# Performance work log

Hardware: AMD Instinct MI355X
Metric: run time of the kernel (lower is better)

Reference implementation:

```python
import jax, jax.numpy as jnp
import numpy as np

B, L, H, NH = 4, 1024, 768, 12
NE, M, P = 30, 6, 600
EMB, BS, NC = 768, 16, 97
NEG = -1e30


def setup_inputs() -> dict:
    key = jax.random.key(0)
    ks = jax.random.split(key, 9)
    sequence_output = jax.random.normal(ks[0], (B, L, H), jnp.float32)
    attention = jax.random.uniform(ks[1], (B, NH, L, L), jnp.float32)
    mention_idx = jax.random.randint(ks[2], (B, NE, M), 0, L)
    mention_mask = jnp.ones((B, NE, M), jnp.float32)
    hts = jax.random.randint(ks[3], (B, P, 2), 0, NE)
    s = 0.02
    head_W = jax.random.normal(ks[4], (EMB, 2 * H), jnp.float32) * s
    head_b = jnp.zeros((EMB,), jnp.float32)
    tail_W = jax.random.normal(ks[5], (EMB, 2 * H), jnp.float32) * s
    tail_b = jnp.zeros((EMB,), jnp.float32)
    proj_W = jax.random.normal(ks[6], (H, EMB * BS), jnp.float32) * s
    cls_W = jax.random.normal(ks[7], (NC, H), jnp.float32) * s
    cls_b = jnp.zeros((NC,), jnp.float32)
    return {
        'sequence_output': sequence_output, 'attention': attention,
        'head_W': head_W, 'head_b': head_b, 'tail_W': tail_W, 'tail_b': tail_b,
        'proj_W': proj_W, 'cls_W': cls_W, 'cls_b': cls_b,
        'mention_mask': mention_mask, 'mention_idx': mention_idx, 'hts': hts,
    }


def reference(sequence_output, attention, head_W, head_b, tail_W, tail_b,
              proj_W, cls_W, cls_b, mention_mask, mention_idx, hts):
    b_, l_, h_ = sequence_output.shape
    bidx = jnp.arange(b_)[:, None, None]                     # [B,1,1]
    # ---- per-entity pooling (segment reduce over ragged mentions) ----
    m_emb = sequence_output[bidx, mention_idx]               # [B,NE,M,H]
    att_t = attention.transpose(0, 2, 1, 3)                  # [B,L,NH,L]
    m_att = att_t[bidx, mention_idx]                         # [B,NE,M,NH,L]
    masked = jnp.where(mention_mask[..., None] > 0, m_emb, NEG)
    e_emb = jax.nn.logsumexp(masked, axis=2)                 # [B,NE,H]
    cnt = jnp.maximum(mention_mask.sum(2), 1.0)              # [B,NE]
    e_att = (m_att * mention_mask[..., None, None]).sum(2) / cnt[..., None, None]  # [B,NE,NH,L]
    # ---- head/tail gathers over pairs ----
    b2 = jnp.arange(b_)[:, None]                             # [B,1]
    h_emb = e_emb[b2, hts[..., 0]]                           # [B,P,H]
    t_emb = e_emb[b2, hts[..., 1]]
    h_att = e_att[b2, hts[..., 0]]                           # [B,P,NH,L]
    t_att = e_att[b2, hts[..., 1]]
    ht_att = (h_att * t_att).mean(2)                         # [B,P,L]
    ht_att = ht_att / (ht_att.sum(-1, keepdims=True) + 1e-30)
    rs = jnp.einsum('bpl,blh->bph', ht_att, sequence_output) # [B,P,H]
    # ---- extractors + block-bilinear classifier ----
    hs = jnp.tanh(jnp.concatenate([h_emb, rs], -1) @ head_W.T + head_b)  # [B,P,EMB]
    ts = jnp.tanh(jnp.concatenate([t_emb, rs], -1) @ tail_W.T + tail_b)
    emb = hs.shape[-1]
    bs = proj_W.shape[1] // emb
    p_ = hs.shape[1]
    b1 = hs.reshape(b_, p_, emb // bs, bs)
    b2t = ts.reshape(b_, p_, emb // bs, bs)
    bl = (b1[..., :, None] * b2t[..., None, :]).reshape(b_, p_, emb * bs)
    logits = (bl @ proj_W.T) @ cls_W.T + cls_b               # [B,P,NC]
    return logits
```

## Files before the change

### kernel.cpp

```cpp
#include <hip/hip_runtime.h>
#include <cmath>

#define B_   4
#define L_   1024
#define H_   768
#define NH_  12
#define NE_  30
#define M_   6
#define P_   600
#define EMB_ 768
#define BS_  16
#define NC_  97

typedef __bf16 bf16x8 __attribute__((ext_vector_type(8)));
typedef float floatx4 __attribute__((ext_vector_type(4)));

union V16 { uint4 q; __bf16 b[8]; bf16x8 v; };
union V8  { unsigned long long u; __bf16 b[4]; };

__device__ __forceinline__ void gemm_core(
    const __bf16* __restrict__ A, int lda, long aRow0,
    const __bf16* __restrict__ Bt, int ldb, long bRow0,
    int K, __bf16* sm, floatx4 acc[2][2])
{
  const int tid = threadIdx.x;
  const int lid = tid & 63, w = tid >> 6;
  const int ar = (w & 1) * 32, bc = (w >> 1) * 32;
  const int frow = lid & 15, kg = lid >> 4;
  __bf16* As = sm;
  __bf16* Bs = sm + 64*40;
  const int srow = tid >> 2, skq = (tid & 3) * 8;
  const __bf16* ag = A + (aRow0 + srow) * (long)lda + skq;
  const __bf16* bg = Bt + (bRow0 + srow) * (long)ldb + skq;
  for (int k0 = 0; k0 < K; k0 += 32) {
    uint4 av = *reinterpret_cast<const uint4*>(ag + k0);
    uint4 bv = *reinterpret_cast<const uint4*>(bg + k0);
    __syncthreads();
    *reinterpret_cast<uint4*>(As + srow*40 + skq) = av;
    *reinterpret_cast<uint4*>(Bs + srow*40 + skq) = bv;
    __syncthreads();
    V16 a0, a1, b0, b1;
    a0.q = *reinterpret_cast<const uint4*>(As + (ar + frow)*40 + kg*8);
    a1.q = *reinterpret_cast<const uint4*>(As + (ar + 16 + frow)*40 + kg*8);
    b0.q = *reinterpret_cast<const uint4*>(Bs + (bc + frow)*40 + kg*8);
    b1.q = *reinterpret_cast<const uint4*>(Bs + (bc + 16 + frow)*40 + kg*8);
    acc[0][0] = __builtin_amdgcn_mfma_f32_16x16x32_bf16(a0.v, b0.v, acc[0][0], 0, 0, 0);
    acc[0][1] = __builtin_amdgcn_mfma_f32_16x16x32_bf16(a0.v, b1.v, acc[0][1], 0, 0, 0);
    acc[1][0] = __builtin_amdgcn_mfma_f32_16x16x32_bf16(a1.v, b0.v, acc[1][0], 0, 0, 0);
    acc[1][1] = __builtin_amdgcn_mfma_f32_16x16x32_bf16(a1.v, b1.v, acc[1][1], 0, 0, 0);
  }
}

#define S1_CVT  2400
#define S1_TPW  9216
#define S1_TPS  3072
#define S1_POOL 120
#define S1_ATT  1440

__device__ __forceinline__ void transpose_body(
    const float* __restrict__ in, __bf16* __restrict__ out,
    int R, int C, int bx, int by, float (*t)[33])
{
  int c0 = bx*32, r0 = by*32;
  int tx = threadIdx.x & 31, ty = threadIdx.x >> 5;
#pragma unroll
  for (int p = 0; p < 4; ++p)
    t[ty + p*8][tx] = in[(long)(r0 + ty + p*8)*C + c0 + tx];
  __syncthreads();
#pragma unroll
  for (int p = 0; p < 4; ++p)
    out[(long)(c0 + ty + p*8)*R + r0 + tx] = (__bf16)t[tx][ty + p*8];
}

__global__ __launch_bounds__(256) void k_prep(
    const float* __restrict__ seq, const float* __restrict__ att,
    const float* __restrict__ headW, const float* __restrict__ tailW,
    const float* __restrict__ projW, const float* __restrict__ clsW,
    const float* __restrict__ mmask, const int* __restrict__ midx,
    __bf16* __restrict__ Wt, __bf16* __restrict__ clsA,
    __bf16* __restrict__ projWT, __bf16* __restrict__ seqT,
    __bf16* __restrict__ e_embB, __bf16* __restrict__ e_att)
{
  __shared__ float t[32][33];
  int blk = blockIdx.x;
  int tid = threadIdx.x;
  if (blk < S1_CVT) {
    int gid = blk*256 + tid;
    if (gid < 2*H_*384) {
      int sel = gid / (H_*384);
      int rem = gid % (H_*384);
      int o = rem / 384;
      int k4 = (rem % 384) * 4;
      const float* W = sel ? tailW : headW;
      float4 v = *reinterpret_cast<const float4*>(W + (long)o*(2*H_) + k4);
      V8 d; d.b[0]=(__bf16)v.x; d.b[1]=(__bf16)v.y; d.b[2]=(__bf16)v.z; d.b[3]=(__bf16)v.w;
      *reinterpret_cast<unsigned long long*>(Wt + ((long)sel*H_ + o)*(2*H_) + k4) = d.u;
    } else {
      int rem = gid - 2*H_*384;
      int row = rem / 192;
      int k4 = (rem % 192) * 4;
      V8 d;
      if (row < NC_) {
        float4 v = *reinterpret_cast<const float4*>(clsW + (long)row*H_ + k4);
        d.b[0]=(__bf16)v.x; d.b[1]=(__bf16)v.y; d.b[2]=(__bf16)v.z; d.b[3]=(__bf16)v.w;
      } else {
        d.b[0]=d.b[1]=d.b[2]=d.b[3]=(__bf16)0.f;
      }
      *reinterpret_cast<unsigned long long*>(clsA + (long)row*H_ + k4) = d.u;
    }
  } else if (blk < S1_CVT + S1_TPW) {
    int b = blk - S1_CVT;
    transpose_body(projW, projWT, H_, EMB_*BS_, b % 384, b / 384, t);
  } else if (blk < S1_CVT + S1_TPW + S1_TPS) {
    int b = blk - (S1_CVT + S1_TPW);
    int bx = b % 24, by = (b / 24) % 32, bz = b / (24*32);
    transpose_body(seq + (long)bz*L_*H_, seqT + (long)bz*H_*L_, L_, H_, bx, by, t);
  } else if (blk < S1_CVT + S1_TPW + S1_TPS + S1_POOL) {
    int be = blk - (S1_CVT + S1_TPW + S1_TPS);
    int idx[M_]; float msk[M_];
#pragma unroll
    for (int m = 0; m < M_; ++m) {
      idx[m] = midx[be * M_ + m];
      msk[m] = mmask[be * M_ + m];
    }
    int b = be / NE_;
    const float* sb = seq + (size_t)b * L_ * H_;
    for (int h = tid; h < H_; h += 256) {
      float v[M_]; float mx = -3.0e38f;
#pragma unroll
      for (int m = 0; m < M_; ++m) {
        float x = (msk[m] > 0.f) ? sb[(size_t)idx[m] * H_ + h] : -1e30f;
        v[m] = x; mx = fmaxf(mx, x);
      }
      float s = 0.f;
#pragma unroll
      for (int m = 0; m < M_; ++m) s += expf(v[m] - mx);
      e_embB[(size_t)be * H_ + h] = (__bf16)(mx + logf(s));
    }
  } else {
    int i = (blk - (S1_CVT + S1_TPW + S1_TPS + S1_POOL))*256 + tid;
    int l4 = (i & 255) * 4;
    int nh = (i >> 8) % NH_;
    int be = i / (256 * NH_);
    int b  = be / NE_;
    float s0=0.f, s1=0.f, s2=0.f, s3=0.f, cnt=0.f;
#pragma unroll
    for (int m = 0; m < M_; ++m) {
      float mk = mmask[be*M_ + m];
      cnt += mk;
      int id = midx[be*M_ + m];
      float4 a = *reinterpret_cast<const float4*>(
          att + (((size_t)b*NH_ + nh)*L_ + id)*L_ + l4);
      s0 += mk*a.x; s1 += mk*a.y; s2 += mk*a.z; s3 += mk*a.w;
    }
    float inv = 1.f / fmaxf(cnt, 1.f);
    V8 o;
    o.b[0]=(__bf16)(s0*inv); o.b[1]=(__bf16)(s1*inv);
    o.b[2]=(__bf16)(s2*inv); o.b[3]=(__bf16)(s3*inv);
    *reinterpret_cast<unsigned long long*>(e_att + ((size_t)be*NH_ + nh)*L_ + l4) = o.u;
  }
}

#define S2_WC  384
#define S2_HT  2400
#define S2_PRE 48

__global__ __launch_bounds__(256) void k_mid(
    const __bf16* __restrict__ clsA, const __bf16* __restrict__ projWT,
    const __bf16* __restrict__ e_att, const int* __restrict__ hts,
    const __bf16* __restrict__ e_embB, const __bf16* __restrict__ Wt,
    __bf16* __restrict__ WcT, __bf16* __restrict__ htatt,
    float* __restrict__ hpre, float* __restrict__ tpre)
{
  __shared__ __bf16 sm[2*64*40];
  int blk = blockIdx.x;
  int tid = threadIdx.x;
  if (blk < S2_WC) {
    int n0 = (blk % 192)*64, r0 = (blk / 192)*64;
    floatx4 acc[2][2] = {};
    gemm_core(clsA, H_, r0, projWT, H_, n0, H_, sm, acc);
    int lid = tid & 63, w = tid >> 6;
    int ar = (w&1)*32, bc = (w>>1)*32, frow = lid&15, kg = lid>>4;
#pragma unroll
    for (int i = 0; i < 2; ++i)
#pragma unroll
      for (int r = 0; r < 4; ++r) {
        int c = r0 + ar + i*16 + kg*4 + r;
#pragma unroll
        for (int j = 0; j < 2; ++j)
          WcT[(long)c*(EMB_*BS_) + n0 + bc + j*16 + frow] = (__bf16)acc[i][j][r];
      }
  } else if (blk < S2_WC + S2_HT) {
    int bp = blk - S2_WC;
    int b = bp / P_;
    int hi = hts[bp*2 + 0], ti = hts[bp*2 + 1];
    const __bf16* ha = e_att + (size_t)(b*NE_ + hi) * NH_ * L_;
    const __bf16* ta = e_att + (size_t)(b*NE_ + ti) * NH_ * L_;
    int l4 = tid * 4;
    float v[4] = {0.f,0.f,0.f,0.f};
#pragma unroll
    for (int nh = 0; nh < NH_; ++nh) {
      V8 x, y;
      x.u = *reinterpret_cast<const unsigned long long*>(ha + nh*L_ + l4);
      y.u = *reinterpret_cast<const unsigned long long*>(ta + nh*L_ + l4);
#pragma unroll
      for (int q = 0; q < 4; ++q) v[q] += (float)x.b[q] * (float)y.b[q];
    }
    float loc = 0.f;
#pragma unroll
    for (int q = 0; q < 4; ++q) { v[q] *= (1.f/NH_); loc += v[q]; }
    float* red = reinterpret_cast<float*>(sm);
    for (int off = 32; off > 0; off >>= 1) loc += __shfl_down(loc, off, 64);
    if ((tid & 63) == 0) red[tid >> 6] = loc;
    __syncthreads();
    float inv = 1.f / (red[0] + red[1] + red[2] + red[3] + 1e-30f);
    V8 o;
#pragma unroll
    for (int q = 0; q < 4; ++q) o.b[q] = (__bf16)(v[q] * inv);
    *reinterpret_cast<unsigned long long*>(htatt + (size_t)bp*L_ + l4) = o.u;
  } else {
    int tb = blk - (S2_WC + S2_HT);
    int o0 = (tb % 12)*64;
    int r0 = ((tb / 12) & 1)*64;
    int sel = tb / 24;
    floatx4 acc[2][2] = {};
    gemm_core(e_embB, H_, r0, Wt + (long)sel*H_*(2*H_), 2*H_, o0, H_, sm, acc);
    float* out = sel ? tpre : hpre;
    int lid = tid & 63, w = tid >> 6;
    int ar = (w&1)*32, bc = (w>>1)*32, frow = lid&15, kg = lid>>4;
#pragma unroll
    for (int i = 0; i < 2; ++i)
#pragma unroll
      for (int r = 0; r < 4; ++r) {
        int be = r0 + ar + i*16 + kg*4 + r;
        if (be < B_*NE_) {
#pragma unroll
          for (int j = 0; j < 2; ++j)
            out[(long)be*EMB_ + o0 + bc + j*16 + frow] = acc[i][j][r];
        }
      }
  }
}

__global__ __launch_bounds__(256) void k_rs_mfma(
    const __bf16* __restrict__ htatt, const __bf16* __restrict__ seqT,
    __bf16* __restrict__ rs)
{
  __shared__ __bf16 sm[2*64*40];
  int b = blockIdx.z, p0 = blockIdx.y*64, h0 = blockIdx.x*64;
  floatx4 acc[2][2] = {};
  gemm_core(htatt, L_, (long)b*P_ + p0, seqT + (long)b*H_*L_, L_, h0, L_, sm, acc);
  int lid = threadIdx.x & 63, w = threadIdx.x >> 6;
  int ar = (w&1)*32, bc = (w>>1)*32, frow = lid&15, kg = lid>>4;
#pragma unroll
  for (int i = 0; i < 2; ++i)
#pragma unroll
    for (int r = 0; r < 4; ++r) {
      int p = p0 + ar + i*16 + kg*4 + r;
      if (p < P_) {
#pragma unroll
        for (int j = 0; j < 2; ++j)
          rs[((long)b*P_ + p)*H_ + h0 + bc + j*16 + frow] = (__bf16)acc[i][j][r];
      }
    }
}

__global__ __launch_bounds__(256) void k_extract_mfma(
    const __bf16* __restrict__ rs, const __bf16* __restrict__ Wt,
    const float* __restrict__ headb, const float* __restrict__ tailb,
    const float* __restrict__ hpre, const float* __restrict__ tpre,
    const int* __restrict__ hts, __bf16* __restrict__ hs, __bf16* __restrict__ ts)
{
  __shared__ __bf16 sm[2*64*40];
  int sel = blockIdx.z, r0 = blockIdx.y*64, o0 = blockIdx.x*64;
  const float* bias = sel ? tailb : headb;
  const float* pre = sel ? tpre : hpre;
  __bf16* out = sel ? ts : hs;
  floatx4 acc[2][2] = {};
  gemm_core(rs, H_, r0, Wt + (long)sel*H_*(2*H_) + H_, 2*H_, o0, H_, sm, acc);
  int lid = threadIdx.x & 63, w = threadIdx.x >> 6;
  int ar = (w&1)*32, bc = (w>>1)*32, frow = lid&15, kg = lid>>4;
#pragma unroll
  for (int i = 0; i < 2; ++i)
#pragma unroll
    for (int r = 0; r < 4; ++r) {
      int row = r0 + ar + i*16 + kg*4 + r;
      if (row < B_*P_) {
        int b = row / P_;
        int e = hts[row*2 + sel];
        const float* prow = pre + (long)(b*NE_ + e) * EMB_;
#pragma unroll
        for (int j = 0; j < 2; ++j) {
          int o = o0 + bc + j*16 + frow;
          out[(long)row*EMB_ + o] = (__bf16)tanhf(acc[i][j][r] + prow[o] + bias[o]);
        }
      }
    }
}

__global__ __launch_bounds__(512) void k_logits_mfma(
    const __bf16* __restrict__ hs, const __bf16* __restrict__ ts,
    const __bf16* __restrict__ WcT, const float* __restrict__ clsb,
    float* __restrict__ out)
{
  int r0 = blockIdx.x * 16;
  int tid = threadIdx.x;
  int w = tid >> 6, lid = tid & 63;
  int frow = lid & 15, kg = lid >> 4;
  int row = r0 + frow;
  long hsrow = (long)row * EMB_;
  floatx4 acc[7] = {};
  int kbase0 = w*1536;
  for (int s = 0; s < 48; ++s) {
    int kb = kbase0 + s*32 + kg*8;
    int q16 = (kb >> 8) << 4;
    int ii = (kb >> 4) & 15;
    int jj0 = kb & 15;
    float hv = (float)hs[hsrow + q16 + ii];
    V16 tsv; tsv.q = *reinterpret_cast<const uint4*>(ts + hsrow + q16 + jj0);
    bf16x8 af;
#pragma unroll
    for (int j = 0; j < 8; ++j) af[j] = (__bf16)(hv * (float)tsv.b[j]);
#pragma unroll
    for (int f = 0; f < 7; ++f) {
      V16 bv; bv.q = *reinterpret_cast<const uint4*>(WcT + (long)(f*16 + frow)*(EMB_*BS_) + kb);
      acc[f] = __builtin_amdgcn_mfma_f32_16x16x32_bf16(af, bv.v, acc[f], 0, 0, 0);
    }
  }
  __shared__ float red[8][16][112];
#pragma unroll
  for (int f = 0; f < 7; ++f)
#pragma unroll
    for (int r = 0; r < 4; ++r)
      red[w][kg*4 + r][f*16 + frow] = acc[f][r];
  __syncthreads();
  for (int e = tid; e < 16*112; e += 512) {
    int rr = e / 112, cc = e % 112;
    if (cc < NC_) {
      float s = clsb[cc];
#pragma unroll
      for (int ww = 0; ww < 8; ++ww) s += red[ww][rr][cc];
      out[(long)(r0 + rr)*NC_ + cc] = s;
    }
  }
}

extern "C" void kernel_launch(void* const* d_in, const int* in_sizes, int n_in,
                              void* d_out, int out_size, void* d_ws, size_t ws_size,
                              hipStream_t stream) {
  const float* seq   = (const float*)d_in[0];
  const float* att   = (const float*)d_in[1];
  const float* headW = (const float*)d_in[2];
  const float* headb = (const float*)d_in[3];
  const float* tailW = (const float*)d_in[4];
  const float* tailb = (const float*)d_in[5];
  const float* projW = (const float*)d_in[6];
  const float* clsW  = (const float*)d_in[7];
  const float* clsb  = (const float*)d_in[8];
  const float* mmask = (const float*)d_in[9];
  const int* midx = (const int*)d_in[10];
  const int* hts  = (const int*)d_in[11];

  char* p = (char*)d_ws;
  auto alloc_f = [&](size_t n){ float* r = (float*)p; p += n*sizeof(float); return r; };
  auto alloc_b = [&](size_t n){ __bf16* r = (__bf16*)p; p += n*2; return r; };
  float* hpre    = alloc_f((size_t)B_*NE_*EMB_);
  float* tpre    = alloc_f((size_t)B_*NE_*EMB_);
  __bf16* e_embB = alloc_b((size_t)128*H_);
  __bf16* e_att  = alloc_b((size_t)B_*NE_*NH_*L_);
  __bf16* htattb = alloc_b((size_t)2464*L_);
  __bf16* seqT   = alloc_b((size_t)B_*H_*L_);
  __bf16* rsb    = alloc_b((size_t)2432*H_);
  __bf16* Wt     = alloc_b((size_t)2*H_*2*H_);
  __bf16* clsA   = alloc_b((size_t)128*H_);
  __bf16* WcT    = alloc_b((size_t)128*EMB_*BS_);
  __bf16* projWT = alloc_b((size_t)EMB_*BS_*H_);
  __bf16* hsb = projWT;
  __bf16* tsb = projWT + (size_t)B_*P_*EMB_;

  k_prep<<<S1_CVT + S1_TPW + S1_TPS + S1_POOL + S1_ATT, 256, 0, stream>>>(
      seq, att, headW, tailW, projW, clsW, mmask, midx,
      Wt, clsA, projWT, seqT, e_embB, e_att);
  k_mid<<<S2_WC + S2_HT + S2_PRE, 256, 0, stream>>>(
      clsA, projWT, e_att, hts, e_embB, Wt, WcT, htattb, hpre, tpre);
  k_rs_mfma<<<dim3(H_/64, 10, B_), 256, 0, stream>>>(htattb, seqT, rsb);
  k_extract_mfma<<<dim3(EMB_/64, 38, 2), 256, 0, stream>>>(
      rsb, Wt, headb, tailb, hpre, tpre, hts, hsb, tsb);
  k_logits_mfma<<<150, 512, 0, stream>>>(hsb, tsb, WcT, clsb, (float*)d_out);
}
```

Baseline: 451.7 us.

## Read proj_W directly in Wc GEMM, widen extract tiles, split-K logits

The Wc GEMM now reads the fp32 proj_W with a coalesced row-major load and converts it to bf16 while staging into shared memory. This removes the separate transpose of the 9.4M-element projection matrix and the bf16 copy it produced. The extractor GEMM uses 64x128 tiles so each A tile is reused across twice as many columns. The logits kernel is split across K into two halves, doubling the number of blocks, and a small reduction kernel adds the bias. The trade-off is one extra launch plus a partial-sum buffer, and the Wc GEMM's shared-memory stores are now narrow scalar writes.

```diff
diff --git a/kernel.cpp b/kernel.cpp
--- a/kernel.cpp
+++ b/kernel.cpp
@@ -51,35 +51,95 @@
   }
 }
 
+__device__ __forceinline__ void gemm_core_nn(
+    const __bf16* __restrict__ A, int lda, long aRow0,
+    const float* __restrict__ B, int ldn, int n0,
+    int K, __bf16* sm, floatx4 acc[2][2])
+{
+  const int tid = threadIdx.x;
+  const int lid = tid & 63, w = tid >> 6;
+  const int ar = (w & 1) * 32, bc = (w >> 1) * 32;
+  const int frow = lid & 15, kg = lid >> 4;
+  __bf16* As = sm;
+  __bf16* Bs = sm + 64*40;
+  const int srow = tid >> 2, skq = (tid & 3) * 8;
+  const __bf16* ag = A + (aRow0 + srow) * (long)lda + skq;
+  const int bkk = tid >> 6;
+  const int bnn = tid & 63;
+  for (int k0 = 0; k0 < K; k0 += 32) {
+    uint4 av = *reinterpret_cast<const uint4*>(ag + k0);
+    float bv[8];
+#pragma unroll
+    for (int pass = 0; pass < 8; ++pass)
+      bv[pass] = B[(long)(k0 + pass*4 + bkk)*ldn + n0 + bnn];
+    __syncthreads();
+    *reinterpret_cast<uint4*>(As + srow*40 + skq) = av;
+#pragma unroll
+    for (int pass = 0; pass < 8; ++pass)
+      Bs[bnn*40 + pass*4 + bkk] = (__bf16)bv[pass];
+    __syncthreads();
+    V16 a0, a1, b0, b1;
+    a0.q = *reinterpret_cast<const uint4*>(As + (ar + frow)*40 + kg*8);
+    a1.q = *reinterpret_cast<const uint4*>(As + (ar + 16 + frow)*40 + kg*8);
+    b0.q = *reinterpret_cast<const uint4*>(Bs + (bc + frow)*40 + kg*8);
+    b1.q = *reinterpret_cast<const uint4*>(Bs + (bc + 16 + frow)*40 + kg*8);
+    acc[0][0] = __builtin_amdgcn_mfma_f32_16x16x32_bf16(a0.v, b0.v, acc[0][0], 0, 0, 0);
+    acc[0][1] = __builtin_amdgcn_mfma_f32_16x16x32_bf16(a0.v, b1.v, acc[0][1], 0, 0, 0);
+    acc[1][0] = __builtin_amdgcn_mfma_f32_16x16x32_bf16(a1.v, b0.v, acc[1][0], 0, 0, 0);
+    acc[1][1] = __builtin_amdgcn_mfma_f32_16x16x32_bf16(a1.v, b1.v, acc[1][1], 0, 0, 0);
+  }
+}
+
+__device__ __forceinline__ void gemm_core_wide(
+    const __bf16* __restrict__ A, int lda, long aRow0,
+    const __bf16* __restrict__ Bt, int ldb, long bRow0,
+    int K, __bf16* sm, floatx4 acc[2][4])
+{
+  const int tid = threadIdx.x;
+  const int lid = tid & 63, w = tid >> 6;
+  const int ar = (w & 1) * 32, bc = (w >> 1) * 64;
+  const int frow = lid & 15, kg = lid >> 4;
+  __bf16* As = sm;
+  __bf16* Bs = sm + 64*40;
+  const int srow = tid >> 2, skq = (tid & 3) * 8;
+  const __bf16* ag = A + (aRow0 + srow) * (long)lda + skq;
+  const __bf16* bg0 = Bt + (bRow0 + srow) * (long)ldb + skq;
+  const __bf16* bg1 = Bt + (bRow0 + 64 + srow) * (long)ldb + skq;
+  for (int k0 = 0; k0 < K; k0 += 32) {
+    uint4 av  = *reinterpret_cast<const uint4*>(ag + k0);
+    uint4 bv0 = *reinterpret_cast<const uint4*>(bg0 + k0);
+    uint4 bv1 = *reinterpret_cast<const uint4*>(bg1 + k0);
+    __syncthreads();
+    *reinterpret_cast<uint4*>(As + srow*40 + skq) = av;
+    *reinterpret_cast<uint4*>(Bs + srow*40 + skq) = bv0;
+    *reinterpret_cast<uint4*>(Bs + (64 + srow)*40 + skq) = bv1;
+    __syncthreads();
+    V16 a0, a1;
+    a0.q = *reinterpret_cast<const uint4*>(As + (ar + frow)*40 + kg*8);
+    a1.q = *reinterpret_cast<const uint4*>(As + (ar + 16 + frow)*40 + kg*8);
+#pragma unroll
+    for (int q = 0; q < 4; ++q) {
+      V16 bq;
+      bq.q = *reinterpret_cast<const uint4*>(Bs + (bc + q*16 + frow)*40 + kg*8);
+      acc[0][q] = __builtin_amdgcn_mfma_f32_16x16x32_bf16(a0.v, bq.v, acc[0][q], 0, 0, 0);
+      acc[1][q] = __builtin_amdgcn_mfma_f32_16x16x32_bf16(a1.v, bq.v, acc[1][q], 0, 0, 0);
+    }
+  }
+}
+
 #define S1_CVT  2400
-#define S1_TPW  9216
 #define S1_TPS  3072
 #define S1_POOL 120
 #define S1_ATT  1440
 
-__device__ __forceinline__ void transpose_body(
-    const float* __restrict__ in, __bf16* __restrict__ out,
-    int R, int C, int bx, int by, float (*t)[33])
-{
-  int c0 = bx*32, r0 = by*32;
-  int tx = threadIdx.x & 31, ty = threadIdx.x >> 5;
-#pragma unroll
-  for (int p = 0; p < 4; ++p)
-    t[ty + p*8][tx] = in[(long)(r0 + ty + p*8)*C + c0 + tx];
-  __syncthreads();
-#pragma unroll
-  for (int p = 0; p < 4; ++p)
-    out[(long)(c0 + ty + p*8)*R + r0 + tx] = (__bf16)t[tx][ty + p*8];
-}
-
 __global__ __launch_bounds__(256) void k_prep(
     const float* __restrict__ seq, const float* __restrict__ att,
     const float* __restrict__ headW, const float* __restrict__ tailW,
-    const float* __restrict__ projW, const float* __restrict__ clsW,
+    const float* __restrict__ clsW,
     const float* __restrict__ mmask, const int* __restrict__ midx,
     __bf16* __restrict__ Wt, __bf16* __restrict__ clsA,
-    __bf16* __restrict__ projWT, __bf16* __restrict__ seqT,
-    __bf16* __restrict__ e_embB, __bf16* __restrict__ e_att)
+    __bf16* __restrict__ seqT, __bf16* __restrict__ e_embB,
+    __bf16* __restrict__ e_att)
 {
   __shared__ float t[32][33];
   int blk = blockIdx.x;
@@ -108,15 +168,22 @@
       }
       *reinterpret_cast<unsigned long long*>(clsA + (long)row*H_ + k4) = d.u;
     }
-  } else if (blk < S1_CVT + S1_TPW) {
+  } else if (blk < S1_CVT + S1_TPS) {
     int b = blk - S1_CVT;
-    transpose_body(projW, projWT, H_, EMB_*BS_, b % 384, b / 384, t);
-  } else if (blk < S1_CVT + S1_TPW + S1_TPS) {
-    int b = blk - (S1_CVT + S1_TPW);
     int bx = b % 24, by = (b / 24) % 32, bz = b / (24*32);
-    transpose_body(seq + (long)bz*L_*H_, seqT + (long)bz*H_*L_, L_, H_, bx, by, t);
-  } else if (blk < S1_CVT + S1_TPW + S1_TPS + S1_POOL) {
-    int be = blk - (S1_CVT + S1_TPW + S1_TPS);
+    const float* in = seq + (long)bz*L_*H_;
+    __bf16* out = seqT + (long)bz*H_*L_;
+    int c0 = bx*32, r0 = by*32;
+    int tx = tid & 31, ty = tid >> 5;
+#pragma unroll
+    for (int p = 0; p < 4; ++p)
+      t[ty + p*8][tx] = in[(long)(r0 + ty + p*8)*H_ + c0 + tx];
+    __syncthreads();
+#pragma unroll
+    for (int p = 0; p < 4; ++p)
+      out[(long)(c0 + ty + p*8)*L_ + r0 + tx] = (__bf16)t[tx][ty + p*8];
+  } else if (blk < S1_CVT + S1_TPS + S1_POOL) {
+    int be = blk - (S1_CVT + S1_TPS);
     int idx[M_]; float msk[M_];
 #pragma unroll
     for (int m = 0; m < M_; ++m) {
@@ -138,7 +205,7 @@
       e_embB[(size_t)be * H_ + h] = (__bf16)(mx + logf(s));
     }
   } else {
-    int i = (blk - (S1_CVT + S1_TPW + S1_TPS + S1_POOL))*256 + tid;
+    int i = (blk - (S1_CVT + S1_TPS + S1_POOL))*256 + tid;
     int l4 = (i & 255) * 4;
     int nh = (i >> 8) % NH_;
     int be = i / (256 * NH_);
@@ -166,7 +233,7 @@
 #define S2_PRE 48
 
 __global__ __launch_bounds__(256) void k_mid(
-    const __bf16* __restrict__ clsA, const __bf16* __restrict__ projWT,
+    const __bf16* __restrict__ clsA, const float* __restrict__ projW,
     const __bf16* __restrict__ e_att, const int* __restrict__ hts,
     const __bf16* __restrict__ e_embB, const __bf16* __restrict__ Wt,
     __bf16* __restrict__ WcT, __bf16* __restrict__ htatt,
@@ -178,7 +245,7 @@
   if (blk < S2_WC) {
     int n0 = (blk % 192)*64, r0 = (blk / 192)*64;
     floatx4 acc[2][2] = {};
-    gemm_core(clsA, H_, r0, projWT, H_, n0, H_, sm, acc);
+    gemm_core_nn(clsA, H_, r0, projW, EMB_*BS_, n0, H_, sm, acc);
     int lid = tid & 63, w = tid >> 6;
     int ar = (w&1)*32, bc = (w>>1)*32, frow = lid&15, kg = lid>>4;
 #pragma unroll
@@ -271,15 +338,15 @@
     const float* __restrict__ hpre, const float* __restrict__ tpre,
     const int* __restrict__ hts, __bf16* __restrict__ hs, __bf16* __restrict__ ts)
 {
-  __shared__ __bf16 sm[2*64*40];
-  int sel = blockIdx.z, r0 = blockIdx.y*64, o0 = blockIdx.x*64;
+  __shared__ __bf16 sm[(64+128)*40];
+  int sel = blockIdx.z, r0 = blockIdx.y*64, o0 = blockIdx.x*128;
   const float* bias = sel ? tailb : headb;
   const float* pre = sel ? tpre : hpre;
   __bf16* out = sel ? ts : hs;
-  floatx4 acc[2][2] = {};
-  gemm_core(rs, H_, r0, Wt + (long)sel*H_*(2*H_) + H_, 2*H_, o0, H_, sm, acc);
+  floatx4 acc[2][4] = {};
+  gemm_core_wide(rs, H_, r0, Wt + (long)sel*H_*(2*H_) + H_, 2*H_, o0, H_, sm, acc);
   int lid = threadIdx.x & 63, w = threadIdx.x >> 6;
-  int ar = (w&1)*32, bc = (w>>1)*32, frow = lid&15, kg = lid>>4;
+  int ar = (w&1)*32, bc = (w>>1)*64, frow = lid&15, kg = lid>>4;
 #pragma unroll
   for (int i = 0; i < 2; ++i)
 #pragma unroll
@@ -290,9 +357,9 @@
         int e = hts[row*2 + sel];
         const float* prow = pre + (long)(b*NE_ + e) * EMB_;
 #pragma unroll
-        for (int j = 0; j < 2; ++j) {
-          int o = o0 + bc + j*16 + frow;
-          out[(long)row*EMB_ + o] = (__bf16)tanhf(acc[i][j][r] + prow[o] + bias[o]);
+        for (int q = 0; q < 4; ++q) {
+          int o = o0 + bc + q*16 + frow;
+          out[(long)row*EMB_ + o] = (__bf16)tanhf(acc[i][q][r] + prow[o] + bias[o]);
         }
       }
     }
@@ -300,18 +367,18 @@
 
 __global__ __launch_bounds__(512) void k_logits_mfma(
     const __bf16* __restrict__ hs, const __bf16* __restrict__ ts,
-    const __bf16* __restrict__ WcT, const float* __restrict__ clsb,
-    float* __restrict__ out)
+    const __bf16* __restrict__ WcT, float* __restrict__ partial)
 {
   int r0 = blockIdx.x * 16;
+  int kh = blockIdx.y;
   int tid = threadIdx.x;
   int w = tid >> 6, lid = tid & 63;
   int frow = lid & 15, kg = lid >> 4;
   int row = r0 + frow;
   long hsrow = (long)row * EMB_;
   floatx4 acc[7] = {};
-  int kbase0 = w*1536;
-  for (int s = 0; s < 48; ++s) {
+  int kbase0 = kh*6144 + w*768;
+  for (int s = 0; s < 24; ++s) {
     int kb = kbase0 + s*32 + kg*8;
     int q16 = (kb >> 8) << 4;
     int ii = (kb >> 4) & 15;
@@ -336,13 +403,23 @@
   __syncthreads();
   for (int e = tid; e < 16*112; e += 512) {
     int rr = e / 112, cc = e % 112;
-    if (cc < NC_) {
-      float s = clsb[cc];
-#pragma unroll
-      for (int ww = 0; ww < 8; ++ww) s += red[ww][rr][cc];
-      out[(long)(r0 + rr)*NC_ + cc] = s;
-    }
-  }
+    float s = 0.f;
+#pragma unroll
+    for (int ww = 0; ww < 8; ++ww) s += red[ww][rr][cc];
+    partial[((long)kh*B_*P_ + r0 + rr)*112 + cc] = s;
+  }
+}
+
+__global__ __launch_bounds__(256) void k_lred(
+    const float* __restrict__ partial, const float* __restrict__ clsb,
+    float* __restrict__ out)
+{
+  int gid = blockIdx.x*256 + threadIdx.x;
+  if (gid >= B_*P_*112) return;
+  int row = gid / 112, c = gid % 112;
+  if (c < NC_)
+    out[(long)row*NC_ + c] = partial[(long)row*112 + c]
+                           + partial[((long)B_*P_ + row)*112 + c] + clsb[c];
 }
 
 extern "C" void kernel_launch(void* const* d_in, const int* in_sizes, int n_in,
@@ -366,6 +443,7 @@
   auto alloc_b = [&](size_t n){ __bf16* r = (__bf16*)p; p += n*2; return r; };
   float* hpre    = alloc_f((size_t)B_*NE_*EMB_);
   float* tpre    = alloc_f((size_t)B_*NE_*EMB_);
+  float* partial = alloc_f((size_t)2*B_*P_*112);
   __bf16* e_embB = alloc_b((size_t)128*H_);
   __bf16* e_att  = alloc_b((size_t)B_*NE_*NH_*L_);
   __bf16* htattb = alloc_b((size_t)2464*L_);
@@ -374,17 +452,17 @@
   __bf16* Wt     = alloc_b((size_t)2*H_*2*H_);
   __bf16* clsA   = alloc_b((size_t)128*H_);
   __bf16* WcT    = alloc_b((size_t)128*EMB_*BS_);
-  __bf16* projWT = alloc_b((size_t)EMB_*BS_*H_);
-  __bf16* hsb = projWT;
-  __bf16* tsb = projWT + (size_t)B_*P_*EMB_;
-
-  k_prep<<<S1_CVT + S1_TPW + S1_TPS + S1_POOL + S1_ATT, 256, 0, stream>>>(
-      seq, att, headW, tailW, projW, clsW, mmask, midx,
-      Wt, clsA, projWT, seqT, e_embB, e_att);
+  __bf16* hsb    = alloc_b((size_t)2432*EMB_);
+  __bf16* tsb    = alloc_b((size_t)2432*EMB_);
+
+  k_prep<<<S1_CVT + S1_TPS + S1_POOL + S1_ATT, 256, 0, stream>>>(
+      seq, att, headW, tailW, clsW, mmask, midx,
+      Wt, clsA, seqT, e_embB, e_att);
   k_mid<<<S2_WC + S2_HT + S2_PRE, 256, 0, stream>>>(
-      clsA, projWT, e_att, hts, e_embB, Wt, WcT, htattb, hpre, tpre);
+      clsA, projW, e_att, hts, e_embB, Wt, WcT, htattb, hpre, tpre);
   k_rs_mfma<<<dim3(H_/64, 10, B_), 256, 0, stream>>>(htattb, seqT, rsb);
-  k_extract_mfma<<<dim3(EMB_/64, 38, 2), 256, 0, stream>>>(
+  k_extract_mfma<<<dim3(EMB_/128, 38, 2), 256, 0, stream>>>(
       rsb, Wt, headb, tailb, hpre, tpre, hts, hsb, tsb);
-  k_logits_mfma<<<150, 512, 0, stream>>>(hsb, tsb, WcT, clsb, (float*)d_out);
-}
+  k_logits_mfma<<<dim3(150, 2), 512, 0, stream>>>(hsb, tsb, WcT, partial);
+  k_lred<<<(B_*P_*112 + 255)/256, 256, 0, stream>>>(partial, clsb, (float*)d_out);
+}
```

Measured after the change: 453.9 us. No clear change (+0.5%).
